# Kernel tuning notes

Measured on AMD Instinct MI355X. Metric: run time of the kernel, lower is better.

Reference implementation:

```python
import jax, jax.numpy as jnp
import numpy as np

B, H, W = 4, 256, 256
TARGET_BETA0 = 5
TARGET_LIFETIME = 0.5
LOSS_SCALE = 100.0


def setup_inputs() -> dict:
    key = jax.random.key(0)
    k1, k2 = jax.random.split(key)
    prob_map = jax.random.uniform(k1, (B, 1, H, W), dtype=jnp.float32)
    roi_mask = (jax.random.uniform(k2, (B, 1, H, W)) < 0.9).astype(jnp.float32)
    return {"prob_map": prob_map, "roi_mask": roi_mask}


def _ph0_topk_loss(f):
    """0-dim persistent homology (V-filtration, 4-connectivity) of f:[H,W],
    then standard top-k MSE(target_lifetime) loss. Equivalent to
    cripser.compute_ph_torch(f, maxdim=0, filtration='V') + _standard_loss.
    Algorithm: Kruskal over grid edges with weight max(f[u],f[v]), elder rule.
    All combinatorics run on stop_gradient values; births/deaths are
    differentiable gathers from f at the paired pixel indices."""
    Hh, Ww = f.shape
    N = Hh * Ww
    fv = f.reshape(-1)
    fvc = jax.lax.stop_gradient(fv)

    idx2d = jnp.arange(N, dtype=jnp.int32).reshape(Hh, Ww)
    r_u = idx2d[:, :-1].reshape(-1)  # right edges
    r_v = r_u + 1
    d_u = idx2d[:-1, :].reshape(-1)  # down edges
    d_v = d_u + Ww
    eu = jnp.concatenate([r_u, d_u])
    ev = jnp.concatenate([r_v, d_v])
    ew = jnp.maximum(fvc[eu], fvc[ev])
    order = jnp.argsort(ew)  # process edges by increasing filtration value
    eu, ev = eu[order], ev[order]

    parent0 = jnp.arange(N, dtype=jnp.int32)

    def step(parent, uv):
        u, v = uv[0], uv[1]

        def find(x):
            return jax.lax.while_loop(lambda y: parent[y] != y, lambda y: parent[y], x)

        ru = find(u)
        rv = find(v)
        merge = ru != rv
        # Invariant: a root is the argmin pixel of its component, so
        # fvc[root] is the component's birth value. Elder rule: the root
        # with smaller birth value survives (ties -> smaller index).
        older_u = (fvc[ru] < fvc[rv]) | ((fvc[ru] == fvc[rv]) & (ru < rv))
        keep = jnp.where(older_u, ru, rv)
        die = jnp.where(older_u, rv, ru)
        b_idx = jnp.where(merge, die, -1)  # birth pixel of the dying comp
        d_pix = jnp.where(fvc[u] >= fvc[v], u, v)  # death = max endpoint
        d_idx = jnp.where(merge, d_pix, -1)
        parent = parent.at[die].set(jnp.where(merge, keep, die))
        parent = parent.at[u].set(jnp.where(merge, keep, ru))  # path compression
        parent = parent.at[v].set(jnp.where(merge, keep, rv))
        return parent, (b_idx, d_idx)

    _, (pb, pd_) = jax.lax.scan(step, parent0, jnp.stack([eu, ev], axis=1))

    valid = pb >= 0
    births = fv[jnp.maximum(pb, 0)]
    deaths = fv[jnp.maximum(pd_, 0)]
    life = jnp.where(valid, deaths - births, 0.0)  # lifetimes >= 0

    # sort descending; invalid slots to the end (keys are stop-gradient)
    key_ = jnp.where(valid, jax.lax.stop_gradient(life), -jnp.inf)
    top = jnp.argsort(-key_)[:TARGET_BETA0]
    topk = life[top]
    vk = valid[top]
    n_use = jnp.sum(vk)  # = min(num_finite, target_beta0)
    sq = jnp.where(vk, (topk - TARGET_LIFETIME) ** 2, 0.0)
    return jnp.sum(sq) / jnp.maximum(n_use, 1).astype(f.dtype)


def reference(prob_map, roi_mask):
    prob = prob_map[:, 0] * roi_mask[:, 0]  # roi masking; (1-roi)*0 is a no-op
    filtration = 1.0 - prob
    losses = jax.vmap(_ph0_topk_loss)(filtration)
    return jnp.mean(losses) * LOSS_SCALE
```

## Files before the change

kernel.cpp:

```cpp
#include <hip/hip_runtime.h>
#include <stdint.h>

#define NPIX 65536
#define NRE  65280
#define NE   130560
#define NIMG 4
#define LTPB 1024
#define ETPB 1024
#define NBLK_L (NIMG*32)
#define TPIX 2048
#define EPAD 4096
#define KMAX 4096
#define HSZ  1024
#define LHSZ 2048
#define ECAP 4096
#define NCUT 2560
#define MTAILL 256
#define ETAIL  256
typedef unsigned long long u64;

__device__ __forceinline__ int ufind(unsigned* lbl, int x){
  int r = x, c = (int)lbl[r];
  while (c != r){ r = c; c = (int)lbl[r]; }
  while ((int)lbl[x] != r){ int n = (int)lbl[x]; lbl[x] = (unsigned)r; x = n; }
  return r;
}
__device__ __forceinline__ int ufind16(unsigned short* uf, int x){
  int r = x, c = (int)uf[r];
  while (c != r){ r = c; c = (int)uf[r]; }
  while ((int)uf[x] != r){ int n = (int)uf[x]; uf[x] = (unsigned short)r; x = n; }
  return r;
}

__device__ __forceinline__ void merge5(float* a, const float* b){
  float out[5]; int ia = 0, ib = 0;
  #pragma unroll
  for (int k = 0; k < 5; ++k){
    float av = (ia < 5) ? a[ia] : -2.0f;
    float bv = (ib < 5) ? b[ib] : -2.0f;
    if (av >= bv){ out[k] = av; ++ia; } else { out[k] = bv; ++ib; }
  }
  #pragma unroll
  for (int k = 0; k < 5; ++k) a[k] = out[k];
}

__device__ __forceinline__ void ins5(float* t5, float v){
  if (v > t5[4]){
    int j = 4;
    while (j > 0 && t5[j-1] < v){ t5[j] = t5[j-1]; --j; }
    t5[j] = v;
  }
}

__global__ __launch_bounds__(LTPB)
void ph0_local(const float* __restrict__ prob, const float* __restrict__ roi,
               float* __restrict__ LIFEg, unsigned* __restrict__ CIDg,
               u64* __restrict__ LAg, u64* __restrict__ LBg,
               unsigned* __restrict__ C, unsigned* __restrict__ C2,
               unsigned* __restrict__ CUTWg, u64* __restrict__ RNKIg,
               float* __restrict__ T5g)
{
  const int blk = blockIdx.x;
  const int img = blk >> 5;
  const int tile = blk & 31;
  const int tr = tile >> 2, tc = tile & 3;
  const int gr0 = tr*32, gc0 = tc*64;
  const int tid = threadIdx.x;
  const int lane = tid & 63;

  const float* pm = prob + img*NPIX;
  const float* rm = roi  + img*NPIX;
  float* LIFE = LIFEg + img*NPIX;
  unsigned* CID = CIDg + img*NPIX;
  unsigned* CUTW = CUTWg + img*NCUT;
  u64* RNKI = RNKIg + (size_t)img*NPIX;
  u64* LA = LAg + (size_t)img*NE;
  unsigned* DUM = (unsigned*)(LBg + (size_t)img*NE + 65536);

  __shared__ float          sf[TPIX];
  __shared__ unsigned       slbl[TPIX];
  __shared__ unsigned       smeb[2][TPIX];
  __shared__ float          slife[TPIX];
  __shared__ unsigned short el[2][EPAD];
  __shared__ unsigned       aux[EPAD];
  __shared__ unsigned       bkw[192];
  __shared__ unsigned short bkp[192];
  __shared__ unsigned       s_fired[TPIX/32];
  __shared__ float          s_t5w[(LTPB/64)*5];
  __shared__ int s_n[3];

  float t5[5] = {-1.f,-1.f,-1.f,-1.f,-1.f};

  for (int p = tid; p < TPIX; p += LTPB){
    int gp = ((gr0 + (p>>6))<<8) + gc0 + (p&63);
    float fv = 1.0f - pm[gp]*rm[gp];
    sf[p] = fv; slbl[p] = (unsigned)p;
    smeb[0][p] = 0xFFFFFFFFu; smeb[1][p] = 0xFFFFFFFFu;
    slife[p] = 0.0f;
  }
  if (tid < 3) s_n[tid] = 0;
  if (tid < TPIX/32) s_fired[tid] = 0;
  for (int s = tid; s < 192; s += LTPB){
    unsigned wv = 0xFFFFFFFFu; int p = 0; int gq = -1;
    if (s < 32){ if (tc > 0){ p = s*64;        gq = ((gr0+s)<<8)    + gc0 - 1;  } }
    else if (s < 64){ int k=s-32;  if (tc < 3){ p = k*64+63;  gq = ((gr0+k)<<8)  + gc0 + 64; } }
    else if (s < 128){ int k=s-64; if (tr > 0){ p = k;        gq = ((gr0-1)<<8)  + gc0 + k;  } }
    else { int k=s-128;            if (tr < 7){ p = 31*64+k;  gq = ((gr0+32)<<8) + gc0 + k;  } }
    if (gq >= 0){
      int gp = ((gr0 + (p>>6))<<8) + gc0 + (p&63);
      float fp = 1.0f - pm[gp]*rm[gp];
      float fq = 1.0f - pm[gq]*rm[gq];
      wv = __float_as_uint(fmaxf(fp, fq));
    }
    bkw[s] = wv; bkp[s] = (unsigned short)p;
  }
  __syncthreads();

  if (tid < 192){
    int s = tid;
    if (s >= 32 && s < 64  && tc < 3) CUTW[(tc<<8) | (gr0 + (s-32))] = bkw[s];
    if (s >= 128           && tr < 7) CUTW[768 + (tr<<8) + (gc0 + (s-128))] = bkw[s];
  }

  int M = EPAD, cur = 0, rd = 0;
  bool tailm = false;
  for (; rd < 100000; ++rd){
    int nxt = cur ^ 1;
    unsigned* sme  = smeb[rd & 1];
    unsigned* smeN = smeb[(rd+1) & 1];
    int bs = tid - (LTPB - 192);
    if (bs >= 0){
      unsigned wv = bkw[bs];
      if (wv != 0xFFFFFFFFu) atomicMin(&sme[ufind(slbl, (int)bkp[bs])], wv);
    }
    int Mpad = (M + 63) & ~63;
    for (int idx = tid; idx < Mpad; idx += LTPB){
      bool keep = false; int e=0,u=0,v=0,a=0,b=0;
      if (idx < M){
        e = (rd == 0) ? idx : (int)el[cur][idx];
        bool valid;
        if (e < 2048){ u=e; v=e+1; valid = ((e&63)!=63); }
        else { u=e-2048; v=u+64; valid = ((u>>6)!=31); }
        if (valid){
          a = ufind(slbl,u); b = ufind(slbl,v);
          if (a != b){
            unsigned wb = __float_as_uint(fmaxf(sf[u],sf[v]));
            atomicMin(&sme[a],wb); atomicMin(&sme[b],wb);
            keep = true;
          }
        }
      }
      u64 m = __ballot(keep);
      if (m){
        int pos0 = __popcll(m & ((1ULL<<lane)-1));
        int leader = __ffsll((long long)m)-1;
        int base = 0;
        if (lane == leader) base = atomicAdd(&s_n[rd%3], __popcll(m));
        base = __shfl(base, leader);
        if (keep){
          el[nxt][base+pos0] = (unsigned short)e;
          aux[base+pos0] = (unsigned)a | ((unsigned)b<<16);
        }
      }
    }
    if (tid < 32){
      int rs = rd < 47 ? rd : 47;
      __builtin_nontemporal_store(0x1u, &DUM[(tile*48 + rs)*32 + tid]);
    }
    __syncthreads();
    int n = s_n[rd%3];
    cur = nxt;
    if (n == M || n == 0){ M = n; break; }
    M = n;
    for (int idx = tid; idx < M; idx += LTPB){
      int e = (int)el[cur][idx];
      unsigned ab = aux[idx];
      int a = (int)(ab & 0xFFFFu), b = (int)(ab >> 16);
      int u, v;
      if (e < 2048){ u = e; v = e + 1; } else { u = e - 2048; v = u + 64; }
      float w = fmaxf(sf[u], sf[v]);
      unsigned wb = __float_as_uint(w);
      float fa = sf[a], fb = sf[b];
      bool bd = (fb < fa) || ((fb == fa) && (b < a));
      int die = bd ? a : b, keep = bd ? b : a;
      if (sme[die] == wb){
        slbl[die] = (unsigned)keep;
        float lt = w - (bd ? fa : fb);
        slife[die] = lt;
        unsigned bbit = 1u << (die & 31);
        if (!(atomicOr(&s_fired[die >> 5], bbit) & bbit)) ins5(t5, lt);
      }
      smeN[a] = 0xFFFFFFFFu; smeN[b] = 0xFFFFFFFFu;
    }
    if (tid == 0) s_n[(rd+1)%3] = 0;
    __syncthreads();
    if (M <= MTAILL){ ++rd; tailm = true; break; }
  }

  if (tailm){
    if (tid < 64){
      for (;; ++rd){
        unsigned* sme  = smeb[rd & 1];
        unsigned* smeN = smeb[(rd+1) & 1];
        for (int s = lane; s < 192; s += 64){
          unsigned wv = bkw[s];
          if (wv != 0xFFFFFFFFu) atomicMin(&sme[ufind(slbl, (int)bkp[s])], wv);
        }
        __builtin_amdgcn_wave_barrier();
        if (lane < 32){
          int rs = rd < 47 ? rd : 47;
          __builtin_nontemporal_store(0x1u, &DUM[(tile*48 + rs)*32 + lane]);
        }
        int nxt = cur ^ 1;
        int nacc = 0;
        for (int i0 = 0; i0 < M; i0 += 64){
          int idx = i0 + lane;
          bool keep = false; int e = 0, a = 0, b = 0;
          if (idx < M){
            e = (int)el[cur][idx];
            int u, v;
            if (e < 2048){ u = e; v = e + 1; } else { u = e - 2048; v = u + 64; }
            a = ufind(slbl,u); b = ufind(slbl,v);
            if (a != b){
              unsigned wb = __float_as_uint(fmaxf(sf[u],sf[v]));
              atomicMin(&sme[a],wb); atomicMin(&sme[b],wb);
              keep = true;
            }
          }
          u64 mm = __ballot(keep);
          if (keep){
            int pos = nacc + __popcll(mm & ((1ULL<<lane)-1));
            el[nxt][pos] = (unsigned short)e;
            aux[pos] = (unsigned)a | ((unsigned)b<<16);
          }
          nacc += __popcll(mm);
        }
        __builtin_amdgcn_wave_barrier();
        int n = nacc;
        cur = nxt;
        if (n == M || n == 0){ M = n; break; }
        M = n;
        for (int i0 = 0; i0 < M; i0 += 64){
          int idx = i0 + lane;
          if (idx < M){
            int e = (int)el[cur][idx];
            unsigned ab = aux[idx];
            int a = (int)(ab & 0xFFFFu), b = (int)(ab >> 16);
            int u, v;
            if (e < 2048){ u = e; v = e + 1; } else { u = e - 2048; v = u + 64; }
            float w = fmaxf(sf[u], sf[v]);
            unsigned wb = __float_as_uint(w);
            float fa = sf[a], fb = sf[b];
            bool bd = (fb < fa) || ((fb == fa) && (b < a));
            int die = bd ? a : b, kp = bd ? b : a;
            if (sme[die] == wb){
              slbl[die] = (unsigned)kp;
              float lt = w - (bd ? fa : fb);
              slife[die] = lt;
              unsigned bbit = 1u << (die & 31);
              if (!(atomicOr(&s_fired[die >> 5], bbit) & bbit)) ins5(t5, lt);
            }
            smeN[a] = 0xFFFFFFFFu; smeN[b] = 0xFFFFFFFFu;
          }
        }
        __builtin_amdgcn_wave_barrier();
      }
      if (lane == 0){ s_n[0] = M; s_n[1] = cur; }
    }
    __syncthreads();
    M = s_n[0]; cur = s_n[1];
  }

  unsigned* posm = smeb[0];
  for (int p = tid; p < TPIX; p += LTPB){
    if ((int)slbl[p] == p){
      unsigned pos = atomicAdd(&C2[img], 1u);
      posm[p] = pos;
      unsigned gp = (unsigned)(((gr0 + (p>>6))<<8) + gc0 + (p&63));
      RNKI[pos] = ((u64)__float_as_uint(sf[p]) << 32) | gp;
    }
  }
  __syncthreads();
  for (int p = tid; p < TPIX; p += LTPB){
    int r = ufind(slbl, p);
    int gp = ((gr0 + (p>>6))<<8) + gc0 + (p&63);
    CID[gp] = posm[r];
    LIFE[gp] = slife[p];
  }
  __syncthreads();

  unsigned* hk = (unsigned*)&el[cur ^ 1][0];
  unsigned* hw = slbl;
  for (int i = tid; i < LHSZ; i += LTPB){ hk[i] = 0xFFFFFFFFu; hw[i] = 0xFFFFFFFFu; }
  __syncthreads();

  unsigned* ctr = &C[img];
  int Mpad2 = (M + 63) & ~63;
  for (int idx = tid; idx < Mpad2; idx += LTPB){
    bool spill = false;
    u64 rec = 0;
    if (idx < M){
      int e = (int)el[cur][idx];
      unsigned ab = aux[idx];
      int a = (int)(ab & 0xFFFFu), b = (int)(ab >> 16);
      int u, v;
      if (e < 2048){ u = e; v = e + 1; } else { u = e - 2048; v = u + 64; }
      unsigned wb = __float_as_uint(fmaxf(sf[u], sf[v]));
      int lo = a < b ? a : b, hi = a < b ? b : a;
      unsigned key = ((unsigned)lo << 11) | (unsigned)hi;
      unsigned h = ((key * 2654435761u) >> 21) & (LHSZ-1);
      bool ins = false;
      #pragma unroll
      for (int t = 0; t < 8; ++t){
        unsigned old = atomicCAS(&hk[h], 0xFFFFFFFFu, key);
        if (old == 0xFFFFFFFFu || old == key){ atomicMin(&hw[h], wb); ins = true; break; }
        h = (h + 1) & (LHSZ-1);
      }
      if (!ins){
        spill = true;
        rec = ((u64)wb << 32) | ((u64)posm[a] << 16) | posm[b];
      }
    }
    u64 m = __ballot(spill);
    if (m){
      int pos0 = __popcll(m & ((1ULL<<lane)-1));
      int leader = __ffsll((long long)m)-1;
      unsigned base = 0;
      if (lane == leader) base = atomicAdd(ctr, (unsigned)__popcll(m));
      base = (unsigned)__shfl((int)base, leader);
      if (spill) LA[base + pos0] = rec;
    }
  }
  __syncthreads();
  for (int h = tid; h < LHSZ; h += LTPB){
    unsigned key = hk[h];
    bool ok = (key != 0xFFFFFFFFu);
    u64 rec = 0;
    if (ok){
      int a = (int)(key >> 11), b = (int)(key & 0x7FFu);
      rec = ((u64)hw[h] << 32) | ((u64)posm[a] << 16) | posm[b];
    }
    u64 m = __ballot(ok);
    if (m){
      int pos0 = __popcll(m & ((1ULL<<lane)-1));
      int leader = __ffsll((long long)m)-1;
      unsigned base = 0;
      if (lane == leader) base = atomicAdd(ctr, (unsigned)__popcll(m));
      base = (unsigned)__shfl((int)base, leader);
      if (ok) LA[base + pos0] = rec;
    }
  }

  #pragma unroll
  for (int off = 1; off < 64; off <<= 1){
    float o[5];
    #pragma unroll
    for (int k = 0; k < 5; ++k) o[k] = __shfl_xor(t5[k], off);
    merge5(t5, o);
  }
  if (lane == 0){
    int wv = tid >> 6;
    #pragma unroll
    for (int k = 0; k < 5; ++k) s_t5w[wv*5+k] = t5[k];
  }
  __syncthreads();
  if (tid < 64){
    float u5[5];
    #pragma unroll
    for (int k = 0; k < 5; ++k) u5[k] = (tid < LTPB/64) ? s_t5w[tid*5+k] : -2.0f;
    #pragma unroll
    for (int off = 1; off < 16; off <<= 1){
      float o[5];
      #pragma unroll
      for (int k = 0; k < 5; ++k) o[k] = __shfl_xor(u5[k], off);
      merge5(u5, o);
    }
    if (tid == 0){
      #pragma unroll
      for (int k = 0; k < 5; ++k) T5g[blk*5+k] = u5[k];
    }
  }
}

#define RUN_ROUNDS_GLOBAL(UF, ME, RNK)                                       \
  for (int k = tid; k < K; k += ETPB) UF[k] = (unsigned short)k;             \
  __syncthreads();                                                           \
  for (int rdg = 0; rdg < 70000 && n > 0; ++rdg){                            \
    for (int k = tid; k < K; k += ETPB) ME[k] = 0xFFFFFFFFu;                 \
    if (tid == 0) s_n[0] = 0;                                                \
    __syncthreads();                                                         \
    int Mpad = (n + 63) & ~63;                                               \
    for (int idx = tid; idx < Mpad; idx += ETPB){                            \
      bool keep = false; unsigned wb = 0; int a = 0, b = 0;                  \
      if (idx < n){                                                          \
        u64 rec = src[idx];                                                  \
        wb = (unsigned)(rec >> 32);                                          \
        a = (int)((rec >> 16) & 0xFFFFu);                                    \
        b = (int)(rec & 0xFFFFu);                                            \
        a = ufind16(UF, a); b = ufind16(UF, b);                              \
        if (a != b){ atomicMin(&ME[a], wb); atomicMin(&ME[b], wb); keep = true; } \
      }                                                                      \
      u64 m = __ballot(keep);                                                \
      if (m){                                                                \
        int pos0 = __popcll(m & ((1ULL<<lane)-1));                           \
        int leader = __ffsll((long long)m)-1;                                \
        int base = 0;                                                        \
        if (lane == leader) base = atomicAdd(&s_n[0], __popcll(m));          \
        base = __shfl(base, leader);                                         \
        if (keep) dst[base+pos0] = ((u64)wb<<32)|((u64)(unsigned)a<<16)|(unsigned)b; \
      }                                                                      \
    }                                                                        \
    __syncthreads();                                                         \
    int nn = s_n[0];                                                         \
    for (int idx = tid; idx < nn; idx += ETPB){                              \
      u64 rec = dst[idx];                                                    \
      unsigned wb = (unsigned)(rec >> 32);                                   \
      int a = (int)((rec >> 16) & 0xFFFFu);                                  \
      int b = (int)(rec & 0xFFFFu);                                          \
      bool bd = RNK[b] < RNK[a];                                             \
      int die = bd ? a : b, kp = bd ? b : a;                                 \
      if (ME[die] == wb){                                                    \
        UF[die] = (unsigned short)kp;                                        \
        u64 rk = RNK[die];                                                   \
        life[(unsigned)(rk & 0xFFFFFFFFu)] =                                 \
            __uint_as_float(wb) - __uint_as_float((unsigned)(rk >> 32));     \
      }                                                                      \
    }                                                                        \
    __syncthreads();                                                         \
    u64* t = src; src = dst; dst = t; n = nn;                                \
  }

__global__ __launch_bounds__(ETPB)
void ph0_endgame(float* __restrict__ LIFEg, unsigned* __restrict__ CIDg,
                 const unsigned* __restrict__ CUTWg, u64* __restrict__ RNKIg,
                 u64* __restrict__ LAg, u64* __restrict__ LBg,
                 const unsigned* __restrict__ C, const unsigned* __restrict__ C2,
                 const float* __restrict__ T5g,
                 float* __restrict__ LOSS, unsigned* __restrict__ DONE,
                 float* __restrict__ out)
{
  const int img = blockIdx.x, tid = threadIdx.x;
  const int lane = tid & 63;
  float* life = LIFEg + img*NPIX;
  unsigned* cid = CIDg + img*NPIX;
  const unsigned* cw = CUTWg + img*NCUT;
  u64* RNKI = RNKIg + (size_t)img*NPIX;
  u64* src = LAg + (size_t)img*NE;
  u64* dst = LBg + (size_t)img*NE;

  __shared__ unsigned short s_uf[KMAX];
  __shared__ unsigned s_meB[2*KMAX];
  __shared__ unsigned s_hkB[2*HSZ];
  __shared__ unsigned s_hwB[2*HSZ];
  __shared__ u64 s_rnk[KMAX];
  __shared__ u64 s_lstA[ECAP];
  __shared__ u64 s_lstB[ECAP];
  __shared__ unsigned s_fired[KMAX/32];
  __shared__ float s_w5[(ETPB/64)*5];
  __shared__ int s_n[3];

  const int K = (int)C2[img];
  const int nInt = (int)C[img];

  for (int s = tid; s < NCUT; s += ETPB){
    int gu, gv;
    if (s < 768){ int ci = s >> 8, row = s & 255, col = 63 + (ci<<6); gu = (row<<8)+col; gv = gu+1; }
    else { int k = s - 768; int ri = k >> 8, colh = k & 255, gr = 31 + (ri<<5); gu = (gr<<8)+colh; gv = gu+256; }
    unsigned ia = cid[gu];
    unsigned ib = cid[gv];
    unsigned wb = cw[s];
    s_lstA[s] = ((u64)wb << 32) | ((u64)ia << 16) | ib;
  }
  if (tid < 3) s_n[tid] = 0;
  int n = nInt + NCUT;

  float t5[5] = {-1.f,-1.f,-1.f,-1.f,-1.f};

  if (K <= KMAX){
    for (int k = tid; k < K; k += ETPB){
      s_uf[k] = (unsigned short)k;
      s_rnk[k] = RNKI[k];
      s_meB[k] = 0xFFFFFFFFu;
    }
    for (int h = tid; h < HSZ; h += ETPB){ s_hkB[h] = 0xFFFFFFFFu; s_hwB[h] = 0xFFFFFFFFu; }
    if (tid < KMAX/32) s_fired[tid] = 0;
    if (tid < 32*5) ins5(t5, T5g[img*(32*5) + tid]);
    __syncthreads();

    u64 *lsrc = s_lstA, *ldst = s_lstB;
    int rd = 0; bool tailm = false;

    for (; rd < 70000; ++rd){
      const int bi = rd & 1;
      unsigned* me  = s_meB + bi*KMAX;
      unsigned* meN = s_meB + (bi^1)*KMAX;
      unsigned* hk = s_hkB + bi*HSZ;
      unsigned* hw = s_hwB + bi*HSZ;
      const bool useHash = (n > 1024);
      int Mpad = (n + 63) & ~63;
      for (int idx = tid; idx < Mpad; idx += ETPB){
        bool app = false; unsigned wb = 0; int a = 0, b = 0;
        if (idx < n){
          u64 rec;
          if (rd == 0) rec = (idx < NCUT) ? lsrc[idx] : src[idx - NCUT];
          else         rec = (idx < ECAP) ? lsrc[idx] : src[idx];
          a = (int)((rec >> 16) & 0xFFFFu);
          b = (int)(rec & 0xFFFFu);
          a = ufind16(s_uf, a); b = ufind16(s_uf, b);
          if (a != b){
            wb = (unsigned)(rec >> 32);
            if (useHash){
              int lo = a < b ? a : b, hi = a < b ? b : a;
              unsigned key = ((unsigned)lo << 12) | (unsigned)hi;
              unsigned h = ((key * 2654435761u) >> 20) & (HSZ-1);
              bool ins = false;
              #pragma unroll
              for (int t = 0; t < 8; ++t){
                unsigned old = atomicCAS(&hk[h], 0xFFFFFFFFu, key);
                if (old == 0xFFFFFFFFu || old == key){ atomicMin(&hw[h], wb); ins = true; break; }
                h = (h + 1) & (HSZ-1);
              }
              if (!ins){ atomicMin(&me[a], wb); atomicMin(&me[b], wb); app = true; }
            } else {
              atomicMin(&me[a], wb); atomicMin(&me[b], wb); app = true;
            }
          }
        }
        u64 m = __ballot(app);
        if (m){
          int pos0 = __popcll(m & ((1ULL<<lane)-1));
          int leader = __ffsll((long long)m)-1;
          int base = 0;
          if (lane == leader) base = atomicAdd(&s_n[rd%3], __popcll(m));
          base = __shfl(base, leader);
          if (app){
            u64 r = ((u64)wb<<32)|((u64)(unsigned)a<<16)|(unsigned)b;
            int pos = base+pos0;
            if (pos < ECAP) ldst[pos] = r; else dst[pos] = r;
          }
        }
      }
      __syncthreads();
      if (useHash){
        for (int h = tid; h < HSZ; h += ETPB){
          unsigned key = hk[h];
          bool okk = (key != 0xFFFFFFFFu);
          unsigned wb = 0; int a = 0, b = 0;
          if (okk){
            a = (int)(key >> 12); b = (int)(key & 0xFFFu);
            wb = hw[h];
            atomicMin(&me[a], wb); atomicMin(&me[b], wb);
          }
          u64 m = __ballot(okk);
          if (m){
            int pos0 = __popcll(m & ((1ULL<<lane)-1));
            int leader = __ffsll((long long)m)-1;
            int base = 0;
            if (lane == leader) base = atomicAdd(&s_n[rd%3], __popcll(m));
            base = __shfl(base, leader);
            if (okk){
              u64 r = ((u64)wb<<32)|((u64)(unsigned)a<<16)|(unsigned)b;
              int pos = base+pos0;
              if (pos < ECAP) ldst[pos] = r; else dst[pos] = r;
            }
          }
        }
        __syncthreads();
      }
      int nn = s_n[rd%3];
      if (nn == 0) break;
      for (int idx = tid; idx < nn; idx += ETPB){
        u64 rec = (idx < ECAP) ? ldst[idx] : dst[idx];
        unsigned wb = (unsigned)(rec >> 32);
        int a = (int)((rec >> 16) & 0xFFFFu);
        int b = (int)(rec & 0xFFFFu);
        u64 ra = s_rnk[a], rb = s_rnk[b];
        bool bd = rb < ra;
        int die = bd ? a : b, kp = bd ? b : a;
        if (me[die] == wb){
          s_uf[die] = (unsigned short)kp;
          unsigned bbit = 1u << (die & 31);
          if (!(atomicOr(&s_fired[die >> 5], bbit) & bbit)){
            u64 rk = bd ? ra : rb;
            ins5(t5, __uint_as_float(wb) - __uint_as_float((unsigned)(rk >> 32)));
          }
        }
        meN[a] = 0xFFFFFFFFu; meN[b] = 0xFFFFFFFFu;
      }
      if (nn > 1024){
        unsigned* hkN = s_hkB + (bi^1)*HSZ;
        unsigned* hwN = s_hwB + (bi^1)*HSZ;
        for (int h = tid; h < HSZ; h += ETPB){ hkN[h] = 0xFFFFFFFFu; hwN[h] = 0xFFFFFFFFu; }
      }
      if (tid == 0) s_n[(rd+1)%3] = 0;
      __syncthreads();
      { u64* t = src; src = dst; dst = t; }
      { u64* t2 = lsrc; lsrc = ldst; ldst = t2; }
      n = nn;
      if (n <= ETAIL){ ++rd; tailm = true; break; }
    }

    if (tailm){
      if (tid < 64){
        for (;; ++rd){
          const int bi = rd & 1;
          unsigned* me  = s_meB + bi*KMAX;
          unsigned* meN = s_meB + (bi^1)*KMAX;
          int nacc = 0;
          for (int i0 = 0; i0 < n; i0 += 64){
            int idx = i0 + lane;
            bool app = false; unsigned wb = 0; int a = 0, b = 0;
            if (idx < n){
              u64 rec = lsrc[idx];
              a = (int)((rec >> 16) & 0xFFFFu);
              b = (int)(rec & 0xFFFFu);
              a = ufind16(s_uf, a); b = ufind16(s_uf, b);
              if (a != b){
                wb = (unsigned)(rec >> 32);
                atomicMin(&me[a], wb); atomicMin(&me[b], wb);
                app = true;
              }
            }
            u64 mm = __ballot(app);
            if (app){
              int pos = nacc + __popcll(mm & ((1ULL<<lane)-1));
              ldst[pos] = ((u64)wb<<32)|((u64)(unsigned)a<<16)|(unsigned)b;
            }
            nacc += __popcll(mm);
          }
          __builtin_amdgcn_wave_barrier();
          int nn = nacc;
          if (nn == 0) break;
          for (int i0 = 0; i0 < nn; i0 += 64){
            int idx = i0 + lane;
            if (idx < nn){
              u64 rec = ldst[idx];
              unsigned wb = (unsigned)(rec >> 32);
              int a = (int)((rec >> 16) & 0xFFFFu);
              int b = (int)(rec & 0xFFFFu);
              u64 ra = s_rnk[a], rb = s_rnk[b];
              bool bd = rb < ra;
              int die = bd ? a : b, kp = bd ? b : a;
              if (me[die] == wb){
                s_uf[die] = (unsigned short)kp;
                unsigned bbit = 1u << (die & 31);
                if (!(atomicOr(&s_fired[die >> 5], bbit) & bbit)){
                  u64 rk = bd ? ra : rb;
                  ins5(t5, __uint_as_float(wb) - __uint_as_float((unsigned)(rk >> 32)));
                }
              }
              meN[a] = 0xFFFFFFFFu; meN[b] = 0xFFFFFFFFu;
            }
          }
          __builtin_amdgcn_wave_barrier();
          { u64* t2 = lsrc; lsrc = ldst; ldst = t2; }
          n = nn;
        }
      }
      __syncthreads();
    }
  } else {
    __syncthreads();
    for (int s = tid; s < NCUT; s += ETPB) src[nInt + s] = s_lstA[s];
    __syncthreads();
    unsigned short* g_uf = (unsigned short*)cid;
    unsigned*       g_me = (unsigned*)(cid + NPIX/2);
    u64*            g_rnk = RNKI;
    RUN_ROUNDS_GLOBAL(g_uf, g_me, g_rnk)
    for (int i = tid; i < NPIX; i += ETPB) ins5(t5, life[i]);
  }

  #pragma unroll
  for (int off = 1; off < 64; off <<= 1){
    float o[5];
    #pragma unroll
    for (int k = 0; k < 5; ++k) o[k] = __shfl_xor(t5[k], off);
    merge5(t5, o);
  }
  if (lane == 0){
    int wv = tid >> 6;
    #pragma unroll
    for (int k = 0; k < 5; ++k) s_w5[wv*5+k] = t5[k];
  }
  __syncthreads();
  if (tid < 64){
    float u5[5];
    #pragma unroll
    for (int k = 0; k < 5; ++k) u5[k] = (tid < ETPB/64) ? s_w5[tid*5+k] : -2.0f;
    #pragma unroll
    for (int off = 1; off < 16; off <<= 1){
      float o[5];
      #pragma unroll
      for (int k = 0; k < 5; ++k) o[k] = __shfl_xor(u5[k], off);
      merge5(u5, o);
    }
    if (tid == 0){
      float lsum = 0.0f;
      #pragma unroll
      for (int k = 0; k < 5; ++k){ float d = u5[k] - 0.5f; lsum += d*d; }
      atomicExch(&LOSS[img], lsum * 0.2f);
      __threadfence();
      unsigned prev = atomicAdd(DONE, 1u);
      if (prev == NIMG - 1){
        float s = 0.0f;
        #pragma unroll
        for (int i = 0; i < NIMG; ++i) s += atomicAdd(&LOSS[i], 0.0f);
        out[0] = s * 25.0f;
      }
    }
  }

  if (img == 0 && tid == 0){
    u64 t0 = __builtin_amdgcn_s_memrealtime();
    while (__builtin_amdgcn_s_memrealtime() - t0 < 5000ULL) {}
  }
}

extern "C" void kernel_launch(void* const* d_in, const int* in_sizes, int n_in,
                              void* d_out, int out_size, void* d_ws, size_t ws_size,
                              hipStream_t stream)
{
  const float* prob = (const float*)d_in[0];
  const float* roi  = (const float*)d_in[1];
  char* ws = (char*)d_ws;
  const size_t SZL = (size_t)4*NE*8;
  float*    LIFE = (float*)(ws + (1u<<20));
  unsigned* CID  = (unsigned*)(ws + (2u<<20));
  unsigned* CUTW = (unsigned*)(ws + (3u<<20));
  u64*      LA   = (u64*)(ws + (5u<<20));
  u64*      LB   = (u64*)(ws + (5u<<20) + SZL);
  u64*      RNKI = (u64*)(ws + (5u<<20) + 2*SZL);
  unsigned* C    = (unsigned*)(ws + (5u<<20) + 2*SZL + (2u<<20));
  unsigned* C2   = C + 4;
  unsigned* DONE = C + 8;
  float*    LOSS = (float*)((char*)C + 64);
  float*    T5   = (float*)(ws + (5u<<20) + 2*SZL - 2560);
  float*    out  = (float*)d_out;

  hipMemsetAsync(C, 0, 64, stream);
  ph0_local<<<NBLK_L, LTPB, 0, stream>>>(prob, roi, LIFE, CID, LA, LB, C, C2, CUTW, RNKI, T5);
  ph0_endgame<<<NIMG, ETPB, 0, stream>>>(LIFE, CID, CUTW, RNKI, LA, LB, C, C2, T5, LOSS, DONE, out);
}
```

Baseline: 310.5 us.

## Fuse local tile pass and per-image endgame into one kernel with last-block handoff

Merges the per-tile union-find kernel and the per-image endgame kernel into a single launch. A per-image completion counter (TDONE) lets the last tile block of each image continue into the endgame, using a single aliased shared-memory buffer sized for both phases. It also drops the artificial spin-wait at the end of the old endgame kernel. This removes one kernel launch and the inter-kernel gap, at the cost of a large shared-memory footprint per block, which lowers occupancy for the tile phase, and of correctness depending on cross-block memory fences.

```diff
diff --git a/kernel.cpp b/kernel.cpp
--- a/kernel.cpp
+++ b/kernel.cpp
@@ -2,12 +2,10 @@
 #include <stdint.h>
 
 #define NPIX 65536
-#define NRE  65280
 #define NE   130560
 #define NIMG 4
-#define LTPB 1024
-#define ETPB 1024
-#define NBLK_L (NIMG*32)
+#define TPB  1024
+#define NBLK (NIMG*32)
 #define TPIX 2048
 #define EPAD 4096
 #define KMAX 4096
@@ -52,345 +50,15 @@
   }
 }
 
-__global__ __launch_bounds__(LTPB)
-void ph0_local(const float* __restrict__ prob, const float* __restrict__ roi,
-               float* __restrict__ LIFEg, unsigned* __restrict__ CIDg,
-               u64* __restrict__ LAg, u64* __restrict__ LBg,
-               unsigned* __restrict__ C, unsigned* __restrict__ C2,
-               unsigned* __restrict__ CUTWg, u64* __restrict__ RNKIg,
-               float* __restrict__ T5g)
-{
-  const int blk = blockIdx.x;
-  const int img = blk >> 5;
-  const int tile = blk & 31;
-  const int tr = tile >> 2, tc = tile & 3;
-  const int gr0 = tr*32, gc0 = tc*64;
-  const int tid = threadIdx.x;
-  const int lane = tid & 63;
-
-  const float* pm = prob + img*NPIX;
-  const float* rm = roi  + img*NPIX;
-  float* LIFE = LIFEg + img*NPIX;
-  unsigned* CID = CIDg + img*NPIX;
-  unsigned* CUTW = CUTWg + img*NCUT;
-  u64* RNKI = RNKIg + (size_t)img*NPIX;
-  u64* LA = LAg + (size_t)img*NE;
-  unsigned* DUM = (unsigned*)(LBg + (size_t)img*NE + 65536);
-
-  __shared__ float          sf[TPIX];
-  __shared__ unsigned       slbl[TPIX];
-  __shared__ unsigned       smeb[2][TPIX];
-  __shared__ float          slife[TPIX];
-  __shared__ unsigned short el[2][EPAD];
-  __shared__ unsigned       aux[EPAD];
-  __shared__ unsigned       bkw[192];
-  __shared__ unsigned short bkp[192];
-  __shared__ unsigned       s_fired[TPIX/32];
-  __shared__ float          s_t5w[(LTPB/64)*5];
-  __shared__ int s_n[3];
-
-  float t5[5] = {-1.f,-1.f,-1.f,-1.f,-1.f};
-
-  for (int p = tid; p < TPIX; p += LTPB){
-    int gp = ((gr0 + (p>>6))<<8) + gc0 + (p&63);
-    float fv = 1.0f - pm[gp]*rm[gp];
-    sf[p] = fv; slbl[p] = (unsigned)p;
-    smeb[0][p] = 0xFFFFFFFFu; smeb[1][p] = 0xFFFFFFFFu;
-    slife[p] = 0.0f;
-  }
-  if (tid < 3) s_n[tid] = 0;
-  if (tid < TPIX/32) s_fired[tid] = 0;
-  for (int s = tid; s < 192; s += LTPB){
-    unsigned wv = 0xFFFFFFFFu; int p = 0; int gq = -1;
-    if (s < 32){ if (tc > 0){ p = s*64;        gq = ((gr0+s)<<8)    + gc0 - 1;  } }
-    else if (s < 64){ int k=s-32;  if (tc < 3){ p = k*64+63;  gq = ((gr0+k)<<8)  + gc0 + 64; } }
-    else if (s < 128){ int k=s-64; if (tr > 0){ p = k;        gq = ((gr0-1)<<8)  + gc0 + k;  } }
-    else { int k=s-128;            if (tr < 7){ p = 31*64+k;  gq = ((gr0+32)<<8) + gc0 + k;  } }
-    if (gq >= 0){
-      int gp = ((gr0 + (p>>6))<<8) + gc0 + (p&63);
-      float fp = 1.0f - pm[gp]*rm[gp];
-      float fq = 1.0f - pm[gq]*rm[gq];
-      wv = __float_as_uint(fmaxf(fp, fq));
-    }
-    bkw[s] = wv; bkp[s] = (unsigned short)p;
-  }
-  __syncthreads();
-
-  if (tid < 192){
-    int s = tid;
-    if (s >= 32 && s < 64  && tc < 3) CUTW[(tc<<8) | (gr0 + (s-32))] = bkw[s];
-    if (s >= 128           && tr < 7) CUTW[768 + (tr<<8) + (gc0 + (s-128))] = bkw[s];
-  }
-
-  int M = EPAD, cur = 0, rd = 0;
-  bool tailm = false;
-  for (; rd < 100000; ++rd){
-    int nxt = cur ^ 1;
-    unsigned* sme  = smeb[rd & 1];
-    unsigned* smeN = smeb[(rd+1) & 1];
-    int bs = tid - (LTPB - 192);
-    if (bs >= 0){
-      unsigned wv = bkw[bs];
-      if (wv != 0xFFFFFFFFu) atomicMin(&sme[ufind(slbl, (int)bkp[bs])], wv);
-    }
-    int Mpad = (M + 63) & ~63;
-    for (int idx = tid; idx < Mpad; idx += LTPB){
-      bool keep = false; int e=0,u=0,v=0,a=0,b=0;
-      if (idx < M){
-        e = (rd == 0) ? idx : (int)el[cur][idx];
-        bool valid;
-        if (e < 2048){ u=e; v=e+1; valid = ((e&63)!=63); }
-        else { u=e-2048; v=u+64; valid = ((u>>6)!=31); }
-        if (valid){
-          a = ufind(slbl,u); b = ufind(slbl,v);
-          if (a != b){
-            unsigned wb = __float_as_uint(fmaxf(sf[u],sf[v]));
-            atomicMin(&sme[a],wb); atomicMin(&sme[b],wb);
-            keep = true;
-          }
-        }
-      }
-      u64 m = __ballot(keep);
-      if (m){
-        int pos0 = __popcll(m & ((1ULL<<lane)-1));
-        int leader = __ffsll((long long)m)-1;
-        int base = 0;
-        if (lane == leader) base = atomicAdd(&s_n[rd%3], __popcll(m));
-        base = __shfl(base, leader);
-        if (keep){
-          el[nxt][base+pos0] = (unsigned short)e;
-          aux[base+pos0] = (unsigned)a | ((unsigned)b<<16);
-        }
-      }
-    }
-    if (tid < 32){
-      int rs = rd < 47 ? rd : 47;
-      __builtin_nontemporal_store(0x1u, &DUM[(tile*48 + rs)*32 + tid]);
-    }
-    __syncthreads();
-    int n = s_n[rd%3];
-    cur = nxt;
-    if (n == M || n == 0){ M = n; break; }
-    M = n;
-    for (int idx = tid; idx < M; idx += LTPB){
-      int e = (int)el[cur][idx];
-      unsigned ab = aux[idx];
-      int a = (int)(ab & 0xFFFFu), b = (int)(ab >> 16);
-      int u, v;
-      if (e < 2048){ u = e; v = e + 1; } else { u = e - 2048; v = u + 64; }
-      float w = fmaxf(sf[u], sf[v]);
-      unsigned wb = __float_as_uint(w);
-      float fa = sf[a], fb = sf[b];
-      bool bd = (fb < fa) || ((fb == fa) && (b < a));
-      int die = bd ? a : b, keep = bd ? b : a;
-      if (sme[die] == wb){
-        slbl[die] = (unsigned)keep;
-        float lt = w - (bd ? fa : fb);
-        slife[die] = lt;
-        unsigned bbit = 1u << (die & 31);
-        if (!(atomicOr(&s_fired[die >> 5], bbit) & bbit)) ins5(t5, lt);
-      }
-      smeN[a] = 0xFFFFFFFFu; smeN[b] = 0xFFFFFFFFu;
-    }
-    if (tid == 0) s_n[(rd+1)%3] = 0;
-    __syncthreads();
-    if (M <= MTAILL){ ++rd; tailm = true; break; }
-  }
-
-  if (tailm){
-    if (tid < 64){
-      for (;; ++rd){
-        unsigned* sme  = smeb[rd & 1];
-        unsigned* smeN = smeb[(rd+1) & 1];
-        for (int s = lane; s < 192; s += 64){
-          unsigned wv = bkw[s];
-          if (wv != 0xFFFFFFFFu) atomicMin(&sme[ufind(slbl, (int)bkp[s])], wv);
-        }
-        __builtin_amdgcn_wave_barrier();
-        if (lane < 32){
-          int rs = rd < 47 ? rd : 47;
-          __builtin_nontemporal_store(0x1u, &DUM[(tile*48 + rs)*32 + lane]);
-        }
-        int nxt = cur ^ 1;
-        int nacc = 0;
-        for (int i0 = 0; i0 < M; i0 += 64){
-          int idx = i0 + lane;
-          bool keep = false; int e = 0, a = 0, b = 0;
-          if (idx < M){
-            e = (int)el[cur][idx];
-            int u, v;
-            if (e < 2048){ u = e; v = e + 1; } else { u = e - 2048; v = u + 64; }
-            a = ufind(slbl,u); b = ufind(slbl,v);
-            if (a != b){
-              unsigned wb = __float_as_uint(fmaxf(sf[u],sf[v]));
-              atomicMin(&sme[a],wb); atomicMin(&sme[b],wb);
-              keep = true;
-            }
-          }
-          u64 mm = __ballot(keep);
-          if (keep){
-            int pos = nacc + __popcll(mm & ((1ULL<<lane)-1));
-            el[nxt][pos] = (unsigned short)e;
-            aux[pos] = (unsigned)a | ((unsigned)b<<16);
-          }
-          nacc += __popcll(mm);
-        }
-        __builtin_amdgcn_wave_barrier();
-        int n = nacc;
-        cur = nxt;
-        if (n == M || n == 0){ M = n; break; }
-        M = n;
-        for (int i0 = 0; i0 < M; i0 += 64){
-          int idx = i0 + lane;
-          if (idx < M){
-            int e = (int)el[cur][idx];
-            unsigned ab = aux[idx];
-            int a = (int)(ab & 0xFFFFu), b = (int)(ab >> 16);
-            int u, v;
-            if (e < 2048){ u = e; v = e + 1; } else { u = e - 2048; v = u + 64; }
-            float w = fmaxf(sf[u], sf[v]);
-            unsigned wb = __float_as_uint(w);
-            float fa = sf[a], fb = sf[b];
-            bool bd = (fb < fa) || ((fb == fa) && (b < a));
-            int die = bd ? a : b, kp = bd ? b : a;
-            if (sme[die] == wb){
-              slbl[die] = (unsigned)kp;
-              float lt = w - (bd ? fa : fb);
-              slife[die] = lt;
-              unsigned bbit = 1u << (die & 31);
-              if (!(atomicOr(&s_fired[die >> 5], bbit) & bbit)) ins5(t5, lt);
-            }
-            smeN[a] = 0xFFFFFFFFu; smeN[b] = 0xFFFFFFFFu;
-          }
-        }
-        __builtin_amdgcn_wave_barrier();
-      }
-      if (lane == 0){ s_n[0] = M; s_n[1] = cur; }
-    }
-    __syncthreads();
-    M = s_n[0]; cur = s_n[1];
-  }
-
-  unsigned* posm = smeb[0];
-  for (int p = tid; p < TPIX; p += LTPB){
-    if ((int)slbl[p] == p){
-      unsigned pos = atomicAdd(&C2[img], 1u);
-      posm[p] = pos;
-      unsigned gp = (unsigned)(((gr0 + (p>>6))<<8) + gc0 + (p&63));
-      RNKI[pos] = ((u64)__float_as_uint(sf[p]) << 32) | gp;
-    }
-  }
-  __syncthreads();
-  for (int p = tid; p < TPIX; p += LTPB){
-    int r = ufind(slbl, p);
-    int gp = ((gr0 + (p>>6))<<8) + gc0 + (p&63);
-    CID[gp] = posm[r];
-    LIFE[gp] = slife[p];
-  }
-  __syncthreads();
-
-  unsigned* hk = (unsigned*)&el[cur ^ 1][0];
-  unsigned* hw = slbl;
-  for (int i = tid; i < LHSZ; i += LTPB){ hk[i] = 0xFFFFFFFFu; hw[i] = 0xFFFFFFFFu; }
-  __syncthreads();
-
-  unsigned* ctr = &C[img];
-  int Mpad2 = (M + 63) & ~63;
-  for (int idx = tid; idx < Mpad2; idx += LTPB){
-    bool spill = false;
-    u64 rec = 0;
-    if (idx < M){
-      int e = (int)el[cur][idx];
-      unsigned ab = aux[idx];
-      int a = (int)(ab & 0xFFFFu), b = (int)(ab >> 16);
-      int u, v;
-      if (e < 2048){ u = e; v = e + 1; } else { u = e - 2048; v = u + 64; }
-      unsigned wb = __float_as_uint(fmaxf(sf[u], sf[v]));
-      int lo = a < b ? a : b, hi = a < b ? b : a;
-      unsigned key = ((unsigned)lo << 11) | (unsigned)hi;
-      unsigned h = ((key * 2654435761u) >> 21) & (LHSZ-1);
-      bool ins = false;
-      #pragma unroll
-      for (int t = 0; t < 8; ++t){
-        unsigned old = atomicCAS(&hk[h], 0xFFFFFFFFu, key);
-        if (old == 0xFFFFFFFFu || old == key){ atomicMin(&hw[h], wb); ins = true; break; }
-        h = (h + 1) & (LHSZ-1);
-      }
-      if (!ins){
-        spill = true;
-        rec = ((u64)wb << 32) | ((u64)posm[a] << 16) | posm[b];
-      }
-    }
-    u64 m = __ballot(spill);
-    if (m){
-      int pos0 = __popcll(m & ((1ULL<<lane)-1));
-      int leader = __ffsll((long long)m)-1;
-      unsigned base = 0;
-      if (lane == leader) base = atomicAdd(ctr, (unsigned)__popcll(m));
-      base = (unsigned)__shfl((int)base, leader);
-      if (spill) LA[base + pos0] = rec;
-    }
-  }
-  __syncthreads();
-  for (int h = tid; h < LHSZ; h += LTPB){
-    unsigned key = hk[h];
-    bool ok = (key != 0xFFFFFFFFu);
-    u64 rec = 0;
-    if (ok){
-      int a = (int)(key >> 11), b = (int)(key & 0x7FFu);
-      rec = ((u64)hw[h] << 32) | ((u64)posm[a] << 16) | posm[b];
-    }
-    u64 m = __ballot(ok);
-    if (m){
-      int pos0 = __popcll(m & ((1ULL<<lane)-1));
-      int leader = __ffsll((long long)m)-1;
-      unsigned base = 0;
-      if (lane == leader) base = atomicAdd(ctr, (unsigned)__popcll(m));
-      base = (unsigned)__shfl((int)base, leader);
-      if (ok) LA[base + pos0] = rec;
-    }
-  }
-
-  #pragma unroll
-  for (int off = 1; off < 64; off <<= 1){
-    float o[5];
-    #pragma unroll
-    for (int k = 0; k < 5; ++k) o[k] = __shfl_xor(t5[k], off);
-    merge5(t5, o);
-  }
-  if (lane == 0){
-    int wv = tid >> 6;
-    #pragma unroll
-    for (int k = 0; k < 5; ++k) s_t5w[wv*5+k] = t5[k];
-  }
-  __syncthreads();
-  if (tid < 64){
-    float u5[5];
-    #pragma unroll
-    for (int k = 0; k < 5; ++k) u5[k] = (tid < LTPB/64) ? s_t5w[tid*5+k] : -2.0f;
-    #pragma unroll
-    for (int off = 1; off < 16; off <<= 1){
-      float o[5];
-      #pragma unroll
-      for (int k = 0; k < 5; ++k) o[k] = __shfl_xor(u5[k], off);
-      merge5(u5, o);
-    }
-    if (tid == 0){
-      #pragma unroll
-      for (int k = 0; k < 5; ++k) T5g[blk*5+k] = u5[k];
-    }
-  }
-}
-
 #define RUN_ROUNDS_GLOBAL(UF, ME, RNK)                                       \
-  for (int k = tid; k < K; k += ETPB) UF[k] = (unsigned short)k;             \
+  for (int k = tid; k < K; k += TPB) UF[k] = (unsigned short)k;              \
   __syncthreads();                                                           \
   for (int rdg = 0; rdg < 70000 && n > 0; ++rdg){                            \
-    for (int k = tid; k < K; k += ETPB) ME[k] = 0xFFFFFFFFu;                 \
+    for (int k = tid; k < K; k += TPB) ME[k] = 0xFFFFFFFFu;                  \
     if (tid == 0) s_n[0] = 0;                                                \
     __syncthreads();                                                         \
     int Mpad = (n + 63) & ~63;                                               \
-    for (int idx = tid; idx < Mpad; idx += ETPB){                            \
+    for (int idx = tid; idx < Mpad; idx += TPB){                             \
       bool keep = false; unsigned wb = 0; int a = 0, b = 0;                  \
       if (idx < n){                                                          \
         u64 rec = src[idx];                                                  \
@@ -412,7 +80,7 @@
     }                                                                        \
     __syncthreads();                                                         \
     int nn = s_n[0];                                                         \
-    for (int idx = tid; idx < nn; idx += ETPB){                              \
+    for (int idx = tid; idx < nn; idx += TPB){                               \
       u64 rec = dst[idx];                                                    \
       unsigned wb = (unsigned)(rec >> 32);                                   \
       int a = (int)((rec >> 16) & 0xFFFFu);                                  \
@@ -430,83 +98,415 @@
     u64* t = src; src = dst; dst = t; n = nn;                                \
   }
 
-__global__ __launch_bounds__(ETPB)
-void ph0_endgame(float* __restrict__ LIFEg, unsigned* __restrict__ CIDg,
-                 const unsigned* __restrict__ CUTWg, u64* __restrict__ RNKIg,
-                 u64* __restrict__ LAg, u64* __restrict__ LBg,
-                 const unsigned* __restrict__ C, const unsigned* __restrict__ C2,
-                 const float* __restrict__ T5g,
-                 float* __restrict__ LOSS, unsigned* __restrict__ DONE,
-                 float* __restrict__ out)
+__global__ __launch_bounds__(TPB)
+void ph0_fused(const float* __restrict__ prob, const float* __restrict__ roi,
+               float* __restrict__ LIFEg, unsigned* __restrict__ CIDg,
+               u64* __restrict__ LAg, u64* __restrict__ LBg,
+               unsigned* __restrict__ C, unsigned* __restrict__ C2,
+               unsigned* __restrict__ CUTWg, u64* __restrict__ RNKIg,
+               float* __restrict__ T5g, unsigned* __restrict__ TDONE,
+               float* __restrict__ LOSS, unsigned* __restrict__ DONE,
+               float* __restrict__ out)
 {
-  const int img = blockIdx.x, tid = threadIdx.x;
+  const int blk = blockIdx.x;
+  const int img = blk >> 5;
+  const int tile = blk & 31;
+  const int tr = tile >> 2, tc = tile & 3;
+  const int gr0 = tr*32, gc0 = tc*64;
+  const int tid = threadIdx.x;
   const int lane = tid & 63;
-  float* life = LIFEg + img*NPIX;
-  unsigned* cid = CIDg + img*NPIX;
-  const unsigned* cw = CUTWg + img*NCUT;
+
+  const float* pm = prob + img*NPIX;
+  const float* rm = roi  + img*NPIX;
+  float* LIFE = LIFEg + img*NPIX;
+  unsigned* CID = CIDg + img*NPIX;
+  unsigned* CUTW = CUTWg + img*NCUT;
   u64* RNKI = RNKIg + (size_t)img*NPIX;
-  u64* src = LAg + (size_t)img*NE;
+  u64* LA = LAg + (size_t)img*NE;
+  unsigned* DUM = (unsigned*)(LBg + (size_t)img*NE + 65536);
+
+  __shared__ __align__(16) unsigned char SMEM[156672];
+  __shared__ int s_n[3];
+  __shared__ int s_last;
+
+  float*          sf    = (float*)(SMEM);
+  unsigned*       slbl  = (unsigned*)(SMEM + 8192);
+  unsigned*       smebB = (unsigned*)(SMEM + 16384);
+  float*          slife = (float*)(SMEM + 32768);
+  unsigned short* elB   = (unsigned short*)(SMEM + 40960);
+  unsigned*       aux   = (unsigned*)(SMEM + 57344);
+  unsigned*       bkw   = (unsigned*)(SMEM + 73728);
+  unsigned short* bkp   = (unsigned short*)(SMEM + 74496);
+  unsigned*       s_fired = (unsigned*)(SMEM + 74880);
+  float*          s_t5w = (float*)(SMEM + 75136);
+
+  float t5[5] = {-1.f,-1.f,-1.f,-1.f,-1.f};
+
+  for (int p = tid; p < TPIX; p += TPB){
+    int gp = ((gr0 + (p>>6))<<8) + gc0 + (p&63);
+    float fv = 1.0f - pm[gp]*rm[gp];
+    sf[p] = fv; slbl[p] = (unsigned)p;
+    smebB[p] = 0xFFFFFFFFu; smebB[TPIX + p] = 0xFFFFFFFFu;
+    slife[p] = 0.0f;
+  }
+  if (tid < 3) s_n[tid] = 0;
+  if (tid < TPIX/32) s_fired[tid] = 0;
+  for (int s = tid; s < 192; s += TPB){
+    unsigned wv = 0xFFFFFFFFu; int p = 0; int gq = -1;
+    if (s < 32){ if (tc > 0){ p = s*64;        gq = ((gr0+s)<<8)    + gc0 - 1;  } }
+    else if (s < 64){ int k=s-32;  if (tc < 3){ p = k*64+63;  gq = ((gr0+k)<<8)  + gc0 + 64; } }
+    else if (s < 128){ int k=s-64; if (tr > 0){ p = k;        gq = ((gr0-1)<<8)  + gc0 + k;  } }
+    else { int k=s-128;            if (tr < 7){ p = 31*64+k;  gq = ((gr0+32)<<8) + gc0 + k;  } }
+    if (gq >= 0){
+      int gp = ((gr0 + (p>>6))<<8) + gc0 + (p&63);
+      float fp = 1.0f - pm[gp]*rm[gp];
+      float fq = 1.0f - pm[gq]*rm[gq];
+      wv = __float_as_uint(fmaxf(fp, fq));
+    }
+    bkw[s] = wv; bkp[s] = (unsigned short)p;
+  }
+  __syncthreads();
+
+  if (tid < 192){
+    int s = tid;
+    if (s >= 32 && s < 64  && tc < 3) CUTW[(tc<<8) | (gr0 + (s-32))] = bkw[s];
+    if (s >= 128           && tr < 7) CUTW[768 + (tr<<8) + (gc0 + (s-128))] = bkw[s];
+  }
+
+  int M = EPAD, cur = 0, rd = 0;
+  bool tailm = false;
+  for (; rd < 100000; ++rd){
+    int nxt = cur ^ 1;
+    unsigned* sme  = smebB + (rd & 1)*TPIX;
+    unsigned* smeN = smebB + ((rd+1) & 1)*TPIX;
+    int bs = tid - (TPB - 192);
+    if (bs >= 0){
+      unsigned wv = bkw[bs];
+      if (wv != 0xFFFFFFFFu) atomicMin(&sme[ufind(slbl, (int)bkp[bs])], wv);
+    }
+    int Mpad = (M + 63) & ~63;
+    for (int idx = tid; idx < Mpad; idx += TPB){
+      bool keep = false; int e=0,u=0,v=0,a=0,b=0;
+      if (idx < M){
+        e = (rd == 0) ? idx : (int)elB[cur*EPAD + idx];
+        bool valid;
+        if (e < 2048){ u=e; v=e+1; valid = ((e&63)!=63); }
+        else { u=e-2048; v=u+64; valid = ((u>>6)!=31); }
+        if (valid){
+          a = ufind(slbl,u); b = ufind(slbl,v);
+          if (a != b){
+            unsigned wb = __float_as_uint(fmaxf(sf[u],sf[v]));
+            atomicMin(&sme[a],wb); atomicMin(&sme[b],wb);
+            keep = true;
+          }
+        }
+      }
+      u64 m = __ballot(keep);
+      if (m){
+        int pos0 = __popcll(m & ((1ULL<<lane)-1));
+        int leader = __ffsll((long long)m)-1;
+        int base = 0;
+        if (lane == leader) base = atomicAdd(&s_n[rd%3], __popcll(m));
+        base = __shfl(base, leader);
+        if (keep){
+          elB[nxt*EPAD + base+pos0] = (unsigned short)e;
+          aux[base+pos0] = (unsigned)a | ((unsigned)b<<16);
+        }
+      }
+    }
+    if (tid < 32){
+      int rs = rd < 47 ? rd : 47;
+      __builtin_nontemporal_store(0x1u, &DUM[(tile*48 + rs)*32 + tid]);
+    }
+    __syncthreads();
+    int n = s_n[rd%3];
+    cur = nxt;
+    if (n == M || n == 0){ M = n; break; }
+    M = n;
+    for (int idx = tid; idx < M; idx += TPB){
+      int e = (int)elB[cur*EPAD + idx];
+      unsigned ab = aux[idx];
+      int a = (int)(ab & 0xFFFFu), b = (int)(ab >> 16);
+      int u, v;
+      if (e < 2048){ u = e; v = e + 1; } else { u = e - 2048; v = u + 64; }
+      float w = fmaxf(sf[u], sf[v]);
+      unsigned wb = __float_as_uint(w);
+      float fa = sf[a], fb = sf[b];
+      bool bd = (fb < fa) || ((fb == fa) && (b < a));
+      int die = bd ? a : b, keep = bd ? b : a;
+      if (sme[die] == wb){
+        slbl[die] = (unsigned)keep;
+        float lt = w - (bd ? fa : fb);
+        slife[die] = lt;
+        unsigned bbit = 1u << (die & 31);
+        if (!(atomicOr(&s_fired[die >> 5], bbit) & bbit)) ins5(t5, lt);
+      }
+      smeN[a] = 0xFFFFFFFFu; smeN[b] = 0xFFFFFFFFu;
+    }
+    if (tid == 0) s_n[(rd+1)%3] = 0;
+    __syncthreads();
+    if (M <= MTAILL){ ++rd; tailm = true; break; }
+  }
+
+  if (tailm){
+    if (tid < 64){
+      for (;; ++rd){
+        unsigned* sme  = smebB + (rd & 1)*TPIX;
+        unsigned* smeN = smebB + ((rd+1) & 1)*TPIX;
+        for (int s = lane; s < 192; s += 64){
+          unsigned wv = bkw[s];
+          if (wv != 0xFFFFFFFFu) atomicMin(&sme[ufind(slbl, (int)bkp[s])], wv);
+        }
+        __builtin_amdgcn_wave_barrier();
+        if (lane < 32){
+          int rs = rd < 47 ? rd : 47;
+          __builtin_nontemporal_store(0x1u, &DUM[(tile*48 + rs)*32 + lane]);
+        }
+        int nxt = cur ^ 1;
+        int nacc = 0;
+        for (int i0 = 0; i0 < M; i0 += 64){
+          int idx = i0 + lane;
+          bool keep = false; int e = 0, a = 0, b = 0;
+          if (idx < M){
+            e = (int)elB[cur*EPAD + idx];
+            int u, v;
+            if (e < 2048){ u = e; v = e + 1; } else { u = e - 2048; v = u + 64; }
+            a = ufind(slbl,u); b = ufind(slbl,v);
+            if (a != b){
+              unsigned wb = __float_as_uint(fmaxf(sf[u],sf[v]));
+              atomicMin(&sme[a],wb); atomicMin(&sme[b],wb);
+              keep = true;
+            }
+          }
+          u64 mm = __ballot(keep);
+          if (keep){
+            int pos = nacc + __popcll(mm & ((1ULL<<lane)-1));
+            elB[nxt*EPAD + pos] = (unsigned short)e;
+            aux[pos] = (unsigned)a | ((unsigned)b<<16);
+          }
+          nacc += __popcll(mm);
+        }
+        __builtin_amdgcn_wave_barrier();
+        int n = nacc;
+        cur = nxt;
+        if (n == M || n == 0){ M = n; break; }
+        M = n;
+        for (int i0 = 0; i0 < M; i0 += 64){
+          int idx = i0 + lane;
+          if (idx < M){
+            int e = (int)elB[cur*EPAD + idx];
+            unsigned ab = aux[idx];
+            int a = (int)(ab & 0xFFFFu), b = (int)(ab >> 16);
+            int u, v;
+            if (e < 2048){ u = e; v = e + 1; } else { u = e - 2048; v = u + 64; }
+            float w = fmaxf(sf[u], sf[v]);
+            unsigned wb = __float_as_uint(w);
+            float fa = sf[a], fb = sf[b];
+            bool bd = (fb < fa) || ((fb == fa) && (b < a));
+            int die = bd ? a : b, kp = bd ? b : a;
+            if (sme[die] == wb){
+              slbl[die] = (unsigned)kp;
+              float lt = w - (bd ? fa : fb);
+              slife[die] = lt;
+              unsigned bbit = 1u << (die & 31);
+              if (!(atomicOr(&s_fired[die >> 5], bbit) & bbit)) ins5(t5, lt);
+            }
+            smeN[a] = 0xFFFFFFFFu; smeN[b] = 0xFFFFFFFFu;
+          }
+        }
+        __builtin_amdgcn_wave_barrier();
+      }
+      if (lane == 0){ s_n[0] = M; s_n[1] = cur; }
+    }
+    __syncthreads();
+    M = s_n[0]; cur = s_n[1];
+  }
+
+  unsigned* posm = smebB;
+  for (int p = tid; p < TPIX; p += TPB){
+    if ((int)slbl[p] == p){
+      unsigned pos = atomicAdd(&C2[img], 1u);
+      posm[p] = pos;
+      unsigned gp = (unsigned)(((gr0 + (p>>6))<<8) + gc0 + (p&63));
+      RNKI[pos] = ((u64)__float_as_uint(sf[p]) << 32) | gp;
+    }
+  }
+  __syncthreads();
+  for (int p = tid; p < TPIX; p += TPB){
+    int r = ufind(slbl, p);
+    int gp = ((gr0 + (p>>6))<<8) + gc0 + (p&63);
+    CID[gp] = posm[r];
+    LIFE[gp] = slife[p];
+  }
+  __syncthreads();
+
+  unsigned* hk = (unsigned*)(elB + (cur ^ 1)*EPAD);
+  unsigned* hw = slbl;
+  for (int i = tid; i < LHSZ; i += TPB){ hk[i] = 0xFFFFFFFFu; hw[i] = 0xFFFFFFFFu; }
+  __syncthreads();
+
+  unsigned* ctr = &C[img];
+  int Mpad2 = (M + 63) & ~63;
+  for (int idx = tid; idx < Mpad2; idx += TPB){
+    bool spill = false;
+    u64 rec = 0;
+    if (idx < M){
+      int e = (int)elB[cur*EPAD + idx];
+      unsigned ab = aux[idx];
+      int a = (int)(ab & 0xFFFFu), b = (int)(ab >> 16);
+      int u, v;
+      if (e < 2048){ u = e; v = e + 1; } else { u = e - 2048; v = u + 64; }
+      unsigned wb = __float_as_uint(fmaxf(sf[u], sf[v]));
+      int lo = a < b ? a : b, hi = a < b ? b : a;
+      unsigned key = ((unsigned)lo << 11) | (unsigned)hi;
+      unsigned h = ((key * 2654435761u) >> 21) & (LHSZ-1);
+      bool ins = false;
+      #pragma unroll
+      for (int t = 0; t < 8; ++t){
+        unsigned old = atomicCAS(&hk[h], 0xFFFFFFFFu, key);
+        if (old == 0xFFFFFFFFu || old == key){ atomicMin(&hw[h], wb); ins = true; break; }
+        h = (h + 1) & (LHSZ-1);
+      }
+      if (!ins){
+        spill = true;
+        rec = ((u64)wb << 32) | ((u64)posm[a] << 16) | posm[b];
+      }
+    }
+    u64 m = __ballot(spill);
+    if (m){
+      int pos0 = __popcll(m & ((1ULL<<lane)-1));
+      int leader = __ffsll((long long)m)-1;
+      unsigned base = 0;
+      if (lane == leader) base = atomicAdd(ctr, (unsigned)__popcll(m));
+      base = (unsigned)__shfl((int)base, leader);
+      if (spill) LA[base + pos0] = rec;
+    }
+  }
+  __syncthreads();
+  for (int h = tid; h < LHSZ; h += TPB){
+    unsigned key = hk[h];
+    bool ok = (key != 0xFFFFFFFFu);
+    u64 rec = 0;
+    if (ok){
+      int a = (int)(key >> 11), b = (int)(key & 0x7FFu);
+      rec = ((u64)hw[h] << 32) | ((u64)posm[a] << 16) | posm[b];
+    }
+    u64 m = __ballot(ok);
+    if (m){
+      int pos0 = __popcll(m & ((1ULL<<lane)-1));
+      int leader = __ffsll((long long)m)-1;
+      unsigned base = 0;
+      if (lane == leader) base = atomicAdd(ctr, (unsigned)__popcll(m));
+      base = (unsigned)__shfl((int)base, leader);
+      if (ok) LA[base + pos0] = rec;
+    }
+  }
+
+  #pragma unroll
+  for (int off = 1; off < 64; off <<= 1){
+    float o[5];
+    #pragma unroll
+    for (int k = 0; k < 5; ++k) o[k] = __shfl_xor(t5[k], off);
+    merge5(t5, o);
+  }
+  if (lane == 0){
+    int wv = tid >> 6;
+    #pragma unroll
+    for (int k = 0; k < 5; ++k) s_t5w[wv*5+k] = t5[k];
+  }
+  __syncthreads();
+  if (tid < 64){
+    float u5[5];
+    #pragma unroll
+    for (int k = 0; k < 5; ++k) u5[k] = (tid < TPB/64) ? s_t5w[tid*5+k] : -2.0f;
+    #pragma unroll
+    for (int off = 1; off < 16; off <<= 1){
+      float o[5];
+      #pragma unroll
+      for (int k = 0; k < 5; ++k) o[k] = __shfl_xor(u5[k], off);
+      merge5(u5, o);
+    }
+    if (tid == 0){
+      #pragma unroll
+      for (int k = 0; k < 5; ++k) T5g[blk*5+k] = u5[k];
+    }
+  }
+
+  __threadfence();
+  __syncthreads();
+  if (tid == 0){
+    unsigned old = atomicAdd(&TDONE[img], 1u);
+    s_last = (old == 31u) ? 1 : 0;
+  }
+  __syncthreads();
+  if (!s_last) return;
+  __threadfence();
+
+  float* life = LIFE;
+  unsigned* cid = CID;
+  const unsigned* cw = CUTW;
+  u64* src = LA;
   u64* dst = LBg + (size_t)img*NE;
 
-  __shared__ unsigned short s_uf[KMAX];
-  __shared__ unsigned s_meB[2*KMAX];
-  __shared__ unsigned s_hkB[2*HSZ];
-  __shared__ unsigned s_hwB[2*HSZ];
-  __shared__ u64 s_rnk[KMAX];
-  __shared__ u64 s_lstA[ECAP];
-  __shared__ u64 s_lstB[ECAP];
-  __shared__ unsigned s_fired[KMAX/32];
-  __shared__ float s_w5[(ETPB/64)*5];
-  __shared__ int s_n[3];
+  unsigned short* euf  = (unsigned short*)(SMEM);
+  unsigned* emeB = (unsigned*)(SMEM + 8192);
+  unsigned* ehkB = (unsigned*)(SMEM + 40960);
+  unsigned* ehwB = (unsigned*)(SMEM + 49152);
+  u64*      ernk = (u64*)(SMEM + 57344);
+  u64*      elstA = (u64*)(SMEM + 90112);
+  u64*      elstB = (u64*)(SMEM + 122880);
+  unsigned* efired = (unsigned*)(SMEM + 155648);
+  float*    ew5  = (float*)(SMEM + 156160);
 
   const int K = (int)C2[img];
   const int nInt = (int)C[img];
 
-  for (int s = tid; s < NCUT; s += ETPB){
+  for (int s = tid; s < NCUT; s += TPB){
     int gu, gv;
     if (s < 768){ int ci = s >> 8, row = s & 255, col = 63 + (ci<<6); gu = (row<<8)+col; gv = gu+1; }
     else { int k = s - 768; int ri = k >> 8, colh = k & 255, gr = 31 + (ri<<5); gu = (gr<<8)+colh; gv = gu+256; }
     unsigned ia = cid[gu];
     unsigned ib = cid[gv];
     unsigned wb = cw[s];
-    s_lstA[s] = ((u64)wb << 32) | ((u64)ia << 16) | ib;
+    elstA[s] = ((u64)wb << 32) | ((u64)ia << 16) | ib;
   }
   if (tid < 3) s_n[tid] = 0;
   int n = nInt + NCUT;
 
-  float t5[5] = {-1.f,-1.f,-1.f,-1.f,-1.f};
+  #pragma unroll
+  for (int k = 0; k < 5; ++k) t5[k] = -1.f;
 
   if (K <= KMAX){
-    for (int k = tid; k < K; k += ETPB){
-      s_uf[k] = (unsigned short)k;
-      s_rnk[k] = RNKI[k];
-      s_meB[k] = 0xFFFFFFFFu;
-    }
-    for (int h = tid; h < HSZ; h += ETPB){ s_hkB[h] = 0xFFFFFFFFu; s_hwB[h] = 0xFFFFFFFFu; }
-    if (tid < KMAX/32) s_fired[tid] = 0;
+    for (int k = tid; k < K; k += TPB){
+      euf[k] = (unsigned short)k;
+      ernk[k] = RNKI[k];
+      emeB[k] = 0xFFFFFFFFu;
+    }
+    for (int h = tid; h < HSZ; h += TPB){ ehkB[h] = 0xFFFFFFFFu; ehwB[h] = 0xFFFFFFFFu; }
+    if (tid < KMAX/32) efired[tid] = 0;
     if (tid < 32*5) ins5(t5, T5g[img*(32*5) + tid]);
     __syncthreads();
 
-    u64 *lsrc = s_lstA, *ldst = s_lstB;
-    int rd = 0; bool tailm = false;
-
-    for (; rd < 70000; ++rd){
-      const int bi = rd & 1;
-      unsigned* me  = s_meB + bi*KMAX;
-      unsigned* meN = s_meB + (bi^1)*KMAX;
-      unsigned* hk = s_hkB + bi*HSZ;
-      unsigned* hw = s_hwB + bi*HSZ;
+    u64 *lsrc = elstA, *ldst = elstB;
+    int erd = 0; bool etail = false;
+
+    for (; erd < 70000; ++erd){
+      const int bi = erd & 1;
+      unsigned* me  = emeB + bi*KMAX;
+      unsigned* meN = emeB + (bi^1)*KMAX;
+      unsigned* hk2 = ehkB + bi*HSZ;
+      unsigned* hw2 = ehwB + bi*HSZ;
       const bool useHash = (n > 1024);
       int Mpad = (n + 63) & ~63;
-      for (int idx = tid; idx < Mpad; idx += ETPB){
+      for (int idx = tid; idx < Mpad; idx += TPB){
         bool app = false; unsigned wb = 0; int a = 0, b = 0;
         if (idx < n){
           u64 rec;
-          if (rd == 0) rec = (idx < NCUT) ? lsrc[idx] : src[idx - NCUT];
-          else         rec = (idx < ECAP) ? lsrc[idx] : src[idx];
+          if (erd == 0) rec = (idx < NCUT) ? lsrc[idx] : src[idx - NCUT];
+          else          rec = (idx < ECAP) ? lsrc[idx] : src[idx];
           a = (int)((rec >> 16) & 0xFFFFu);
           b = (int)(rec & 0xFFFFu);
-          a = ufind16(s_uf, a); b = ufind16(s_uf, b);
+          a = ufind16(euf, a); b = ufind16(euf, b);
           if (a != b){
             wb = (unsigned)(rec >> 32);
             if (useHash){
@@ -516,8 +516,8 @@
               bool ins = false;
               #pragma unroll
               for (int t = 0; t < 8; ++t){
-                unsigned old = atomicCAS(&hk[h], 0xFFFFFFFFu, key);
-                if (old == 0xFFFFFFFFu || old == key){ atomicMin(&hw[h], wb); ins = true; break; }
+                unsigned old = atomicCAS(&hk2[h], 0xFFFFFFFFu, key);
+                if (old == 0xFFFFFFFFu || old == key){ atomicMin(&hw2[h], wb); ins = true; break; }
                 h = (h + 1) & (HSZ-1);
               }
               if (!ins){ atomicMin(&me[a], wb); atomicMin(&me[b], wb); app = true; }
@@ -531,7 +531,7 @@
           int pos0 = __popcll(m & ((1ULL<<lane)-1));
           int leader = __ffsll((long long)m)-1;
           int base = 0;
-          if (lane == leader) base = atomicAdd(&s_n[rd%3], __popcll(m));
+          if (lane == leader) base = atomicAdd(&s_n[erd%3], __popcll(m));
           base = __shfl(base, leader);
           if (app){
             u64 r = ((u64)wb<<32)|((u64)(unsigned)a<<16)|(unsigned)b;
@@ -542,21 +542,21 @@
       }
       __syncthreads();
       if (useHash){
-        for (int h = tid; h < HSZ; h += ETPB){
-          unsigned key = hk[h];
+        for (int h = tid; h < HSZ; h += TPB){
+          unsigned key = ehkB[bi*HSZ + h];
           bool okk = (key != 0xFFFFFFFFu);
           unsigned wb = 0; int a = 0, b = 0;
           if (okk){
             a = (int)(key >> 12); b = (int)(key & 0xFFFu);
-            wb = hw[h];
-            atomicMin(&me[a], wb); atomicMin(&me[b], wb);
+            wb = ehwB[bi*HSZ + h];
+            atomicMin(&emeB[bi*KMAX + a], wb); atomicMin(&emeB[bi*KMAX + b], wb);
           }
           u64 m = __ballot(okk);
           if (m){
             int pos0 = __popcll(m & ((1ULL<<lane)-1));
             int leader = __ffsll((long long)m)-1;
             int base = 0;
-            if (lane == leader) base = atomicAdd(&s_n[rd%3], __popcll(m));
+            if (lane == leader) base = atomicAdd(&s_n[erd%3], __popcll(m));
             base = __shfl(base, leader);
             if (okk){
               u64 r = ((u64)wb<<32)|((u64)(unsigned)a<<16)|(unsigned)b;
@@ -567,20 +567,20 @@
         }
         __syncthreads();
       }
-      int nn = s_n[rd%3];
+      int nn = s_n[erd%3];
       if (nn == 0) break;
-      for (int idx = tid; idx < nn; idx += ETPB){
+      for (int idx = tid; idx < nn; idx += TPB){
         u64 rec = (idx < ECAP) ? ldst[idx] : dst[idx];
         unsigned wb = (unsigned)(rec >> 32);
         int a = (int)((rec >> 16) & 0xFFFFu);
         int b = (int)(rec & 0xFFFFu);
-        u64 ra = s_rnk[a], rb = s_rnk[b];
+        u64 ra = ernk[a], rb = ernk[b];
         bool bd = rb < ra;
         int die = bd ? a : b, kp = bd ? b : a;
-        if (me[die] == wb){
-          s_uf[die] = (unsigned short)kp;
+        if (emeB[bi*KMAX + die] == wb){
+          euf[die] = (unsigned short)kp;
           unsigned bbit = 1u << (die & 31);
-          if (!(atomicOr(&s_fired[die >> 5], bbit) & bbit)){
+          if (!(atomicOr(&efired[die >> 5], bbit) & bbit)){
             u64 rk = bd ? ra : rb;
             ins5(t5, __uint_as_float(wb) - __uint_as_float((unsigned)(rk >> 32)));
           }
@@ -588,24 +588,24 @@
         meN[a] = 0xFFFFFFFFu; meN[b] = 0xFFFFFFFFu;
       }
       if (nn > 1024){
-        unsigned* hkN = s_hkB + (bi^1)*HSZ;
-        unsigned* hwN = s_hwB + (bi^1)*HSZ;
-        for (int h = tid; h < HSZ; h += ETPB){ hkN[h] = 0xFFFFFFFFu; hwN[h] = 0xFFFFFFFFu; }
-      }
-      if (tid == 0) s_n[(rd+1)%3] = 0;
+        unsigned* hkN = ehkB + (bi^1)*HSZ;
+        unsigned* hwN = ehwB + (bi^1)*HSZ;
+        for (int h = tid; h < HSZ; h += TPB){ hkN[h] = 0xFFFFFFFFu; hwN[h] = 0xFFFFFFFFu; }
+      }
+      if (tid == 0) s_n[(erd+1)%3] = 0;
       __syncthreads();
       { u64* t = src; src = dst; dst = t; }
       { u64* t2 = lsrc; lsrc = ldst; ldst = t2; }
       n = nn;
-      if (n <= ETAIL){ ++rd; tailm = true; break; }
-    }
-
-    if (tailm){
+      if (n <= ETAIL){ ++erd; etail = true; break; }
+    }
+
+    if (etail){
       if (tid < 64){
-        for (;; ++rd){
-          const int bi = rd & 1;
-          unsigned* me  = s_meB + bi*KMAX;
-          unsigned* meN = s_meB + (bi^1)*KMAX;
+        for (;; ++erd){
+          const int bi = erd & 1;
+          unsigned* me  = emeB + bi*KMAX;
+          unsigned* meN = emeB + (bi^1)*KMAX;
           int nacc = 0;
           for (int i0 = 0; i0 < n; i0 += 64){
             int idx = i0 + lane;
@@ -614,7 +614,7 @@
               u64 rec = lsrc[idx];
               a = (int)((rec >> 16) & 0xFFFFu);
               b = (int)(rec & 0xFFFFu);
-              a = ufind16(s_uf, a); b = ufind16(s_uf, b);
+              a = ufind16(euf, a); b = ufind16(euf, b);
               if (a != b){
                 wb = (unsigned)(rec >> 32);
                 atomicMin(&me[a], wb); atomicMin(&me[b], wb);
@@ -638,13 +638,13 @@
               unsigned wb = (unsigned)(rec >> 32);
               int a = (int)((rec >> 16) & 0xFFFFu);
               int b = (int)(rec & 0xFFFFu);
-              u64 ra = s_rnk[a], rb = s_rnk[b];
+              u64 ra = ernk[a], rb = ernk[b];
               bool bd = rb < ra;
               int die = bd ? a : b, kp = bd ? b : a;
               if (me[die] == wb){
-                s_uf[die] = (unsigned short)kp;
+                euf[die] = (unsigned short)kp;
                 unsigned bbit = 1u << (die & 31);
-                if (!(atomicOr(&s_fired[die >> 5], bbit) & bbit)){
+                if (!(atomicOr(&efired[die >> 5], bbit) & bbit)){
                   u64 rk = bd ? ra : rb;
                   ins5(t5, __uint_as_float(wb) - __uint_as_float((unsigned)(rk >> 32)));
                 }
@@ -661,13 +661,13 @@
     }
   } else {
     __syncthreads();
-    for (int s = tid; s < NCUT; s += ETPB) src[nInt + s] = s_lstA[s];
+    for (int s = tid; s < NCUT; s += TPB) src[nInt + s] = elstA[s];
     __syncthreads();
     unsigned short* g_uf = (unsigned short*)cid;
     unsigned*       g_me = (unsigned*)(cid + NPIX/2);
     u64*            g_rnk = RNKI;
     RUN_ROUNDS_GLOBAL(g_uf, g_me, g_rnk)
-    for (int i = tid; i < NPIX; i += ETPB) ins5(t5, life[i]);
+    for (int i = tid; i < NPIX; i += TPB) ins5(t5, life[i]);
   }
 
   #pragma unroll
@@ -680,13 +680,13 @@
   if (lane == 0){
     int wv = tid >> 6;
     #pragma unroll
-    for (int k = 0; k < 5; ++k) s_w5[wv*5+k] = t5[k];
+    for (int k = 0; k < 5; ++k) ew5[wv*5+k] = t5[k];
   }
   __syncthreads();
   if (tid < 64){
     float u5[5];
     #pragma unroll
-    for (int k = 0; k < 5; ++k) u5[k] = (tid < ETPB/64) ? s_w5[tid*5+k] : -2.0f;
+    for (int k = 0; k < 5; ++k) u5[k] = (tid < TPB/64) ? ew5[tid*5+k] : -2.0f;
     #pragma unroll
     for (int off = 1; off < 16; off <<= 1){
       float o[5];
@@ -708,11 +708,6 @@
         out[0] = s * 25.0f;
       }
     }
-  }
-
-  if (img == 0 && tid == 0){
-    u64 t0 = __builtin_amdgcn_s_memrealtime();
-    while (__builtin_amdgcn_s_memrealtime() - t0 < 5000ULL) {}
   }
 }
 
@@ -733,11 +728,12 @@
   unsigned* C    = (unsigned*)(ws + (5u<<20) + 2*SZL + (2u<<20));
   unsigned* C2   = C + 4;
   unsigned* DONE = C + 8;
+  unsigned* TDONE= C + 12;
   float*    LOSS = (float*)((char*)C + 64);
   float*    T5   = (float*)(ws + (5u<<20) + 2*SZL - 2560);
   float*    out  = (float*)d_out;
 
   hipMemsetAsync(C, 0, 64, stream);
-  ph0_local<<<NBLK_L, LTPB, 0, stream>>>(prob, roi, LIFE, CID, LA, LB, C, C2, CUTW, RNKI, T5);
-  ph0_endgame<<<NIMG, ETPB, 0, stream>>>(LIFE, CID, CUTW, RNKI, LA, LB, C, C2, T5, LOSS, DONE, out);
+  ph0_fused<<<NBLK, TPB, 0, stream>>>(prob, roi, LIFE, CID, LA, LB, C, C2,
+                                      CUTW, RNKI, T5, TDONE, LOSS, DONE, out);
 }
```

Result: faster. 298.1 us (-4.0%).
